# Kernel tuning notes

Hardware: AMD Instinct MI355X
Metric: run time of the kernel (lower is better)

## Reference

```python
import jax, jax.numpy as jnp
import numpy as np

B, S, D, N = 16, 1024, 512, 2048
SPECTRAL_RADIUS = 0.95
SPARSITY = 0.01  # effective_sparsity = max(0.01, 5/N) = 0.01 for N=2048


def setup_inputs() -> dict:
    key = jax.random.key(0)
    k_x, k_fb, k_wraw, k_mask, k_win, k_wfb = jax.random.split(key, 6)
    x_seq = jax.random.normal(k_x, (B, S, D), dtype=jnp.float32)
    feedback_seq = jax.random.normal(k_fb, (B, S, D), dtype=jnp.float32)
    initial_state = jnp.zeros((B, N), dtype=jnp.float32)
    # Fixed random reservoir: sparse gaussian rescaled to spectral radius ~0.95.
    # For an NxN gaussian with density p, spectral radius ~= sqrt(N*p), so we
    # rescale by SPECTRAL_RADIUS / sqrt(N*p) (the torch code uses the exact
    # max eigenvalue; this approximation preserves the same math structure).
    W_raw = jax.random.normal(k_wraw, (N, N), dtype=jnp.float32)
    mask = (jax.random.uniform(k_mask, (N, N)) < SPARSITY).astype(jnp.float32)
    W_res = W_raw * mask * (SPECTRAL_RADIUS / jnp.sqrt(N * SPARSITY))
    W_in = jax.random.normal(k_win, (N, D), dtype=jnp.float32) * 0.1
    W_fb = jax.random.normal(k_wfb, (N, D), dtype=jnp.float32) * 0.1
    return {
        "x_seq": x_seq,
        "feedback_seq": feedback_seq,
        "initial_state": initial_state,
        "W_res": W_res,
        "W_in": W_in,
        "W_fb": W_fb,
    }


def reference(x_seq, feedback_seq, initial_state, W_res, W_in, W_fb):
    # Precompute input + feedback projections as one batched GEMM each
    # (same math as per-step einsums: 'bi,ni->bn' == x @ W.T).
    drive = jnp.einsum("bsd,nd->sbn", x_seq, W_in) + jnp.einsum(
        "bsd,nd->sbn", feedback_seq, W_fb
    )  # (S, B, N)

    def step(state, drive_t):
        # pre = state @ W_res.T + W_in x_t + W_fb fb_t
        new_state = jnp.tanh(state @ W_res.T + drive_t)
        return new_state, new_state

    _, states = jax.lax.scan(step, initial_state, drive)  # (S, B, N)
    return jnp.transpose(states, (1, 0, 2))  # (B, S, N)
```

## Files before the change

### kernel.cpp

```cpp
#include <hip/hip_runtime.h>
#include <stdint.h>

typedef unsigned short u16;
typedef unsigned int   u32;
typedef __attribute__((ext_vector_type(8))) short short8;
typedef __attribute__((ext_vector_type(4))) float f32x4;

#define CAP   52
#define CAPW  26

__device__ __forceinline__ u16 rne_bf16(float f){
  u32 u = __float_as_uint(f);
  u32 r = (u + 0x7fffu + ((u >> 16) & 1u)) >> 16;
  return (u16)r;
}
__device__ __forceinline__ float bf16_to_f(u16 h){
  return __uint_as_float(((u32)h) << 16);
}
__device__ __forceinline__ float tanh_fast(float x){
  float e = __expf(2.0f * x);
  return 1.0f - 2.0f / (e + 1.0f);
}

__global__ __launch_bounds__(256) void pack_a_k(const float* __restrict__ x,
                                                const float* __restrict__ fb,
                                                u16* __restrict__ A){
  int idx = blockIdx.x * 256 + threadIdx.x;
  int m = idx >> 9, d = idx & 511;
  float xv = x[idx];
  float fv = fb[idx];
  u16 xh = rne_bf16(xv); u16 xl = rne_bf16(xv - bf16_to_f(xh));
  u16 fh = rne_bf16(fv); u16 fl = rne_bf16(fv - bf16_to_f(fh));
  size_t base = (size_t)m * 2048;
  A[base + d]        = xh;
  A[base + 512 + d]  = fh;
  A[base + 1024 + d] = xl;
  A[base + 1536 + d] = fl;
}

__global__ __launch_bounds__(256) void pack_b_k(const float* __restrict__ Win,
                                                const float* __restrict__ Wfb,
                                                u16* __restrict__ Bm){
  int idx = blockIdx.x * 256 + threadIdx.x;
  int n = idx >> 9, d = idx & 511;
  float iv = Win[idx];
  float fv = Wfb[idx];
  u16 ih = rne_bf16(iv); u16 il = rne_bf16(iv - bf16_to_f(ih));
  u16 fh = rne_bf16(fv); u16 fl = rne_bf16(fv - bf16_to_f(fh));
  size_t base = (size_t)n * 3072;
  Bm[base + d]        = ih;
  Bm[base + 512 + d]  = fh;
  Bm[base + 1024 + d] = ih;
  Bm[base + 1536 + d] = fh;
  Bm[base + 2048 + d] = il;
  Bm[base + 2560 + d] = fl;
}

#define GLDS(gp, lp) __builtin_amdgcn_global_load_lds( \
    (const __attribute__((address_space(1))) void*)(gp), \
    (__attribute__((address_space(3))) void*)(lp), 16, 0, 0)

__global__ __launch_bounds__(256) void gemm_k(const u16* __restrict__ A,
                                              const u16* __restrict__ Bm,
                                              float* __restrict__ C){
  __shared__ __align__(16) u16 As[128 * 32];
  __shared__ __align__(16) u16 Bs[128 * 32];
  const int tid = threadIdx.x;
  const int w = tid >> 6, l = tid & 63;
  const int bid = blockIdx.x;
  const int mt = bid >> 4, nt = bid & 15;
  const int m0 = mt * 128, n0 = nt * 128;
  const int srow = tid >> 2;
  const int scol = (tid & 3) * 8;
  const int wr = w & 1, wc = w >> 1;
  const int lhi = l >> 4, llo = l & 15;

  f32x4 acc[4][4];
  #pragma unroll
  for (int i = 0; i < 4; i++)
    #pragma unroll
    for (int j = 0; j < 4; j++)
      acc[i][j] = (f32x4){0.f, 0.f, 0.f, 0.f};

  for (int kt = 0; kt < 96; ++kt){
    int k = kt * 32;
    int keff = (k >= 2048) ? (k - 2048) : k;
    #pragma unroll
    for (int r = 0; r < 2; r++){
      const u16* ga = A  + (size_t)(m0 + r * 64 + srow) * 2048 + keff + scol;
      GLDS(ga, &As[r * 2048 + w * 512]);
      const u16* gb = Bm + (size_t)(n0 + r * 64 + srow) * 3072 + k + scol;
      GLDS(gb, &Bs[r * 2048 + w * 512]);
    }
    __syncthreads();
    short8 af[4], bf[4];
    #pragma unroll
    for (int i = 0; i < 4; i++){
      af[i] = *(const short8*)&As[(wr * 64 + i * 16 + llo) * 32 + lhi * 8];
      bf[i] = *(const short8*)&Bs[(wc * 64 + i * 16 + llo) * 32 + lhi * 8];
    }
    #pragma unroll
    for (int i = 0; i < 4; i++)
      #pragma unroll
      for (int j = 0; j < 4; j++)
        acc[i][j] = __builtin_amdgcn_mfma_f32_16x16x32_bf16(af[i], bf[j], acc[i][j], 0, 0, 0);
    __syncthreads();
  }
  #pragma unroll
  for (int i = 0; i < 4; i++)
    #pragma unroll
    for (int j = 0; j < 4; j++)
      #pragma unroll
      for (int rg = 0; rg < 4; rg++){
        int mr = m0 + wr * 64 + i * 16 + lhi * 4 + rg;
        int nc = n0 + wc * 64 + j * 16 + llo;
        C[(size_t)mr * 2048 + nc] = acc[i][j][rg];
      }
}

__global__ __launch_bounds__(256) void count_k(const float* __restrict__ W,
                                               int* __restrict__ nnz){
  int gt = blockIdx.x * 256 + threadIdx.x;
  int row = gt >> 6, l = gt & 63;
  const float* wr = W + (size_t)row * 2048;
  int c = 0;
  for (int i = 0; i < 32; i++) c += (wr[i * 64 + l] != 0.0f) ? 1 : 0;
  for (int off = 32; off; off >>= 1) c += __shfl_down(c, off, 64);
  if (l == 0) nnz[row] = c;
}

__global__ __launch_bounds__(1024) void sort_k(const int* __restrict__ nnz,
                                               u32* __restrict__ rowsp,
                                               int* __restrict__ L1a){
  __shared__ int hist[64], off[64], cur[64];
  __shared__ int order[2048];
  int tid = threadIdx.x;
  if (tid < 64){ hist[tid] = 0; cur[tid] = 0; }
  __syncthreads();
  for (int r = tid; r < 2048; r += 1024){
    int b = nnz[r]; if (b > 63) b = 63;
    atomicAdd(&hist[b], 1);
  }
  __syncthreads();
  if (tid == 0){
    int run = 0;
    for (int b = 63; b >= 0; b--){ off[b] = run; run += hist[b]; }
  }
  __syncthreads();
  for (int r = tid; r < 2048; r += 1024){
    int b = nnz[r]; if (b > 63) b = 63;
    int pos = off[b] + atomicAdd(&cur[b], 1);
    order[pos] = r;
  }
  __syncthreads();
  int rA = order[tid], rB = order[2047 - tid];
  rowsp[tid] = (u32)rA | ((u32)rB << 16);
  L1a[tid] = nnz[rA];
}

__global__ __launch_bounds__(256) void fill_k(const float* __restrict__ W,
                                              const u32* __restrict__ rowsp,
                                              float* __restrict__ valw,
                                              u32* __restrict__ col32){
  int gt = blockIdx.x * 256 + threadIdx.x;
  int p = gt >> 6, l = gt & 63;
  u32 rp = rowsp[p];
  int rA = (int)(rp & 0xffffu), rB = (int)(rp >> 16);
  int base = 0;
  for (int h = 0; h < 2; h++){
    int row = h ? rB : rA;
    const float* wr = W + (size_t)row * 2048;
    int cnt = 0;
    for (int i = 0; i < 32; i++){
      int c = i * 64 + l;
      float v = wr[c];
      unsigned long long m = __ballot(v != 0.0f);
      int pre = __popcll(m & ((1ull << l) - 1ull));
      if (v != 0.0f){
        int s = base + cnt + pre;
        if (s < CAP){
          valw[s * 1024 + p] = v;
          col32[s * 1024 + p] = (u32)c;
        }
      }
      cnt += __popcll(m);
    }
    base += cnt;
  }
  for (int s = base + l; s < CAP; s += 64){
    valw[s * 1024 + p] = 0.0f;
    col32[s * 1024 + p] = 0u;
  }
}

__global__ __launch_bounds__(256) void packc_k(const u32* __restrict__ c32,
                                               u32* __restrict__ cw){
  int idx = blockIdx.x * 256 + threadIdx.x;
  int j = idx >> 10, p = idx & 1023;
  cw[j * 1024 + p] = (c32[(2 * j) * 1024 + p] & 0xffffu) | (c32[(2 * j + 1) * 1024 + p] << 16);
}

__global__ __launch_bounds__(1024) void rnn_k(float* __restrict__ out,
                                              const float* __restrict__ init,
                                              const float* __restrict__ valw,
                                              const u32* __restrict__ cwg,
                                              const u32* __restrict__ rowsp,
                                              const int* __restrict__ L1a){
  const int tid = threadIdx.x, b = blockIdx.x;
  float val[CAP]; u32 cw[CAPW];
  #pragma unroll
  for (int k = 0; k < CAP; k++) val[k] = valw[k * 1024 + tid];
  #pragma unroll
  for (int j = 0; j < CAPW; j++) cw[j] = cwg[j * 1024 + tid];
  u32 rp = rowsp[tid];
  int rA = (int)(rp & 0xffffu), rB = (int)(rp >> 16);
  int L1 = L1a[tid];

  __shared__ float st[2048];
  st[tid]        = init[(size_t)b * 2048 + tid];
  st[tid + 1024] = init[(size_t)b * 2048 + tid + 1024];
  __syncthreads();

  float* ob = out + (size_t)b * 1024 * 2048;
  for (int t = 0; t < 1024; t++){
    float* orow = ob + (size_t)t * 2048;
    float dA = orow[rA];
    float dB = orow[rB];
    float aAll = 0.f, aA = 0.f;
    #pragma unroll
    for (int k = 0; k < CAP; k++){
      u32 col = (k & 1) ? (cw[k >> 1] >> 16) : (cw[k >> 1] & 0xffffu);
      float pv = val[k] * st[col];
      aAll += pv;
      aA += (k < L1) ? pv : 0.0f;
    }
    float aB = aAll - aA;
    __syncthreads();
    float sA = tanh_fast(aA + dA);
    float sB = tanh_fast(aB + dB);
    st[rA] = sA; st[rB] = sB;
    __syncthreads();
    orow[rA] = sA;
    orow[rB] = sB;
  }
}

extern "C" void kernel_launch(void* const* d_in, const int* in_sizes, int n_in,
                              void* d_out, int out_size, void* d_ws, size_t ws_size,
                              hipStream_t stream) {
  const float* x    = (const float*)d_in[0];
  const float* fb   = (const float*)d_in[1];
  const float* init = (const float*)d_in[2];
  const float* Wres = (const float*)d_in[3];
  const float* Win  = (const float*)d_in[4];
  const float* Wfb  = (const float*)d_in[5];
  float* out = (float*)d_out;

  char* w8 = (char*)d_ws;
  u16*  A_pack = (u16*)(w8);
  u16*  B_pack = (u16*)(w8 + 67108864);
  float* valw  = (float*)(w8 + 79691776);
  u32*  col32  = (u32*) (w8 + 79904768);
  u32*  colw   = (u32*) (w8 + 80117760);
  int*  nnz    = (int*) (w8 + 80224256);
  u32*  rowsp  = (u32*) (w8 + 80232448);
  int*  L1a    = (int*) (w8 + 80236544);

  pack_a_k<<<32768, 256, 0, stream>>>(x, fb, A_pack);
  pack_b_k<<<4096, 256, 0, stream>>>(Win, Wfb, B_pack);
  gemm_k<<<2048, 256, 0, stream>>>(A_pack, B_pack, out);
  count_k<<<512, 256, 0, stream>>>(Wres, nnz);
  sort_k<<<1, 1024, 0, stream>>>(nnz, rowsp, L1a);
  fill_k<<<256, 256, 0, stream>>>(Wres, rowsp, valw, col32);
  packc_k<<<(CAPW * 1024) / 256, 256, 0, stream>>>(col32, colw);
  rnn_k<<<16, 1024, 0, stream>>>(out, init, valw, colw, rowsp, L1a);
}
```

Measured before the change: 3.649 ms.

## Permute GEMM drive columns and bank-sort sparse columns for coalesced RNN access

```diff
diff --git a/kernel.cpp b/kernel.cpp
--- a/kernel.cpp
+++ b/kernel.cpp
@@ -62,6 +62,7 @@
 
 __global__ __launch_bounds__(256) void gemm_k(const u16* __restrict__ A,
                                               const u16* __restrict__ Bm,
+                                              const int* __restrict__ colmap,
                                               float* __restrict__ C){
   __shared__ __align__(16) u16 As[128 * 32];
   __shared__ __align__(16) u16 Bs[128 * 32];
@@ -106,6 +107,9 @@
         acc[i][j] = __builtin_amdgcn_mfma_f32_16x16x32_bf16(af[i], bf[j], acc[i][j], 0, 0, 0);
     __syncthreads();
   }
+  int cmj[4];
+  #pragma unroll
+  for (int j = 0; j < 4; j++) cmj[j] = colmap[n0 + wc * 64 + j * 16 + llo];
   #pragma unroll
   for (int i = 0; i < 4; i++)
     #pragma unroll
@@ -113,8 +117,7 @@
       #pragma unroll
       for (int rg = 0; rg < 4; rg++){
         int mr = m0 + wr * 64 + i * 16 + lhi * 4 + rg;
-        int nc = n0 + wc * 64 + j * 16 + llo;
-        C[(size_t)mr * 2048 + nc] = acc[i][j][rg];
+        C[(size_t)mr * 2048 + cmj[j]] = acc[i][j][rg];
       }
 }
 
@@ -131,7 +134,8 @@
 
 __global__ __launch_bounds__(1024) void sort_k(const int* __restrict__ nnz,
                                                u32* __restrict__ rowsp,
-                                               int* __restrict__ L1a){
+                                               int* __restrict__ L1a,
+                                               int* __restrict__ colmap){
   __shared__ int hist[64], off[64], cur[64];
   __shared__ int order[2048];
   int tid = threadIdx.x;
@@ -156,6 +160,8 @@
   int rA = order[tid], rB = order[2047 - tid];
   rowsp[tid] = (u32)rA | ((u32)rB << 16);
   L1a[tid] = nnz[rA];
+  colmap[rA] = tid;
+  colmap[rB] = tid + 1024;
 }
 
 __global__ __launch_bounds__(256) void fill_k(const float* __restrict__ W,
@@ -193,19 +199,51 @@
   }
 }
 
-__global__ __launch_bounds__(256) void packc_k(const u32* __restrict__ c32,
-                                               u32* __restrict__ cw){
-  int idx = blockIdx.x * 256 + threadIdx.x;
-  int j = idx >> 10, p = idx & 1023;
-  cw[j * 1024 + p] = (c32[(2 * j) * 1024 + p] & 0xffffu) | (c32[(2 * j + 1) * 1024 + p] << 16);
-}
-
-__global__ __launch_bounds__(1024) void rnn_k(float* __restrict__ out,
-                                              const float* __restrict__ init,
-                                              const float* __restrict__ valw,
-                                              const u32* __restrict__ cwg,
-                                              const u32* __restrict__ rowsp,
-                                              const int* __restrict__ L1a){
+__global__ __launch_bounds__(256) void reorder_k(const float* __restrict__ valw,
+                                                 const u32* __restrict__ col32,
+                                                 const int* __restrict__ L1a,
+                                                 float* __restrict__ val2,
+                                                 u32* __restrict__ cw2){
+  int p = blockIdx.x * 256 + threadIdx.x;
+  float v[CAP]; int c[CAP];
+  float tv[CAP]; int tc[CAP];
+  for (int k = 0; k < CAP; k++){ v[k] = valw[k * 1024 + p]; c[k] = (int)col32[k * 1024 + p]; }
+  int L1 = L1a[p];
+  int lane = p & 63;
+  int b0 = 0;
+  for (int s = 0; s < 2; s++){
+    int b1 = s ? CAP : L1;
+    int len = b1 - b0;
+    if (len > 0){
+      int cnt[32], st_[32], cur[32];
+      for (int b = 0; b < 32; b++){ cnt[b] = 0; cur[b] = 0; }
+      for (int i = b0; i < b1; i++) cnt[c[i] & 31]++;
+      int run = 0;
+      for (int b = 0; b < 32; b++){ st_[b] = run; run += cnt[b]; }
+      for (int i = b0; i < b1; i++){
+        int b = c[i] & 31;
+        int q = st_[b] + (cur[b]++);
+        tv[q] = v[i]; tc[q] = c[i];
+      }
+      int off = (lane * len) >> 6;
+      for (int q = 0; q < len; q++){
+        int src = q + off; if (src >= len) src -= len;
+        v[b0 + q] = tv[src]; c[b0 + q] = tc[src];
+      }
+    }
+    b0 = b1;
+  }
+  for (int k = 0; k < CAP; k++) val2[k * 1024 + p] = v[k];
+  for (int j = 0; j < CAPW; j++)
+    cw2[j * 1024 + p] = ((u32)(c[2 * j] << 2)) | (((u32)(c[2 * j + 1] << 2)) << 16);
+}
+
+__global__ __launch_bounds__(1024, 4) void rnn_k(float* __restrict__ out,
+                                                 const float* __restrict__ init,
+                                                 const float* __restrict__ valw,
+                                                 const u32* __restrict__ cwg,
+                                                 const u32* __restrict__ rowsp,
+                                                 const int* __restrict__ L1a){
   const int tid = threadIdx.x, b = blockIdx.x;
   float val[CAP]; u32 cw[CAPW];
   #pragma unroll
@@ -220,28 +258,31 @@
   st[tid]        = init[(size_t)b * 2048 + tid];
   st[tid + 1024] = init[(size_t)b * 2048 + tid + 1024];
   __syncthreads();
+  const char* stb = (const char*)st;
 
   float* ob = out + (size_t)b * 1024 * 2048;
   for (int t = 0; t < 1024; t++){
     float* orow = ob + (size_t)t * 2048;
-    float dA = orow[rA];
-    float dB = orow[rB];
+    float dA = orow[tid];
+    float dB = orow[tid + 1024];
     float aAll = 0.f, aA = 0.f;
     #pragma unroll
     for (int k = 0; k < CAP; k++){
-      u32 col = (k & 1) ? (cw[k >> 1] >> 16) : (cw[k >> 1] & 0xffffu);
-      float pv = val[k] * st[col];
+      u32 off = (k & 1) ? (cw[k >> 1] >> 16) : (cw[k >> 1] & 0xffffu);
+      float sv = *(const float*)(stb + off);
+      float pv = val[k] * sv;
       aAll += pv;
       aA += (k < L1) ? pv : 0.0f;
     }
-    float aB = aAll - aA;
+    float preA = aA + dA;
+    float preB = (aAll - aA) + dB;
     __syncthreads();
-    float sA = tanh_fast(aA + dA);
-    float sB = tanh_fast(aB + dB);
+    float sA = tanh_fast(preA);
+    float sB = tanh_fast(preB);
     st[rA] = sA; st[rB] = sB;
     __syncthreads();
-    orow[rA] = sA;
-    orow[rB] = sB;
+    orow[tid] = st[tid];
+    orow[tid + 1024] = st[tid + 1024];
   }
 }
 
@@ -261,17 +302,19 @@
   u16*  B_pack = (u16*)(w8 + 67108864);
   float* valw  = (float*)(w8 + 79691776);
   u32*  col32  = (u32*) (w8 + 79904768);
-  u32*  colw   = (u32*) (w8 + 80117760);
-  int*  nnz    = (int*) (w8 + 80224256);
-  u32*  rowsp  = (u32*) (w8 + 80232448);
-  int*  L1a    = (int*) (w8 + 80236544);
+  int*  colmap = (int*) (w8 + 80117760);
+  int*  nnz    = (int*) (w8 + 80125952);
+  u32*  rowsp  = (u32*) (w8 + 80134144);
+  int*  L1a    = (int*) (w8 + 80138240);
+  float* val2  = (float*)(w8);
+  u32*  cw2    = (u32*) (w8 + 212992);
 
   pack_a_k<<<32768, 256, 0, stream>>>(x, fb, A_pack);
   pack_b_k<<<4096, 256, 0, stream>>>(Win, Wfb, B_pack);
-  gemm_k<<<2048, 256, 0, stream>>>(A_pack, B_pack, out);
   count_k<<<512, 256, 0, stream>>>(Wres, nnz);
-  sort_k<<<1, 1024, 0, stream>>>(nnz, rowsp, L1a);
+  sort_k<<<1, 1024, 0, stream>>>(nnz, rowsp, L1a, colmap);
   fill_k<<<256, 256, 0, stream>>>(Wres, rowsp, valw, col32);
-  packc_k<<<(CAPW * 1024) / 256, 256, 0, stream>>>(col32, colw);
-  rnn_k<<<16, 1024, 0, stream>>>(out, init, valw, colw, rowsp, L1a);
-}
+  gemm_k<<<2048, 256, 0, stream>>>(A_pack, B_pack, colmap, out);
+  reorder_k<<<4, 256, 0, stream>>>(valw, col32, L1a, val2, cw2);
+  rnn_k<<<16, 1024, 0, stream>>>(out, init, val2, cw2, rowsp, L1a);
+}
```

Result: slower. 3.810 ms (+4.4%).

## Permute drive GEMM rows, pack weight+column into one word, coalesce recurrent I/O

Applied to the files above, without the earlier changes.

```diff
diff --git a/kernel.cpp b/kernel.cpp
--- a/kernel.cpp
+++ b/kernel.cpp
@@ -7,7 +7,6 @@
 typedef __attribute__((ext_vector_type(4))) float f32x4;
 
 #define CAP   52
-#define CAPW  26
 
 __device__ __forceinline__ u16 rne_bf16(float f){
   u32 u = __float_as_uint(f);
@@ -40,11 +39,13 @@
 
 __global__ __launch_bounds__(256) void pack_b_k(const float* __restrict__ Win,
                                                 const float* __restrict__ Wfb,
+                                                const int* __restrict__ rowperm,
                                                 u16* __restrict__ Bm){
   int idx = blockIdx.x * 256 + threadIdx.x;
   int n = idx >> 9, d = idx & 511;
-  float iv = Win[idx];
-  float fv = Wfb[idx];
+  int row = rowperm[n];
+  float iv = Win[(size_t)row * 512 + d];
+  float fv = Wfb[(size_t)row * 512 + d];
   u16 ih = rne_bf16(iv); u16 il = rne_bf16(iv - bf16_to_f(ih));
   u16 fh = rne_bf16(fv); u16 fl = rne_bf16(fv - bf16_to_f(fh));
   size_t base = (size_t)n * 3072;
@@ -131,7 +132,8 @@
 
 __global__ __launch_bounds__(1024) void sort_k(const int* __restrict__ nnz,
                                                u32* __restrict__ rowsp,
-                                               int* __restrict__ L1a){
+                                               int* __restrict__ L1a,
+                                               int* __restrict__ rowperm){
   __shared__ int hist[64], off[64], cur[64];
   __shared__ int order[2048];
   int tid = threadIdx.x;
@@ -156,12 +158,13 @@
   int rA = order[tid], rB = order[2047 - tid];
   rowsp[tid] = (u32)rA | ((u32)rB << 16);
   L1a[tid] = nnz[rA];
+  rowperm[tid] = rA;
+  rowperm[tid + 1024] = rB;
 }
 
 __global__ __launch_bounds__(256) void fill_k(const float* __restrict__ W,
                                               const u32* __restrict__ rowsp,
-                                              float* __restrict__ valw,
-                                              u32* __restrict__ col32){
+                                              u32* __restrict__ wpk){
   int gt = blockIdx.x * 256 + threadIdx.x;
   int p = gt >> 6, l = gt & 63;
   u32 rp = rowsp[p];
@@ -179,39 +182,30 @@
       if (v != 0.0f){
         int s = base + cnt + pre;
         if (s < CAP){
-          valw[s * 1024 + p] = v;
-          col32[s * 1024 + p] = (u32)c;
+          u32 u = __float_as_uint(v);
+          u = (u + 0x1000u) & 0xFFFFE000u;
+          wpk[s * 1024 + p] = u | ((u32)c << 2);
         }
       }
       cnt += __popcll(m);
     }
     base += cnt;
   }
-  for (int s = base + l; s < CAP; s += 64){
-    valw[s * 1024 + p] = 0.0f;
-    col32[s * 1024 + p] = 0u;
-  }
-}
-
-__global__ __launch_bounds__(256) void packc_k(const u32* __restrict__ c32,
-                                               u32* __restrict__ cw){
-  int idx = blockIdx.x * 256 + threadIdx.x;
-  int j = idx >> 10, p = idx & 1023;
-  cw[j * 1024 + p] = (c32[(2 * j) * 1024 + p] & 0xffffu) | (c32[(2 * j + 1) * 1024 + p] << 16);
-}
-
-__global__ __launch_bounds__(1024) void rnn_k(float* __restrict__ out,
-                                              const float* __restrict__ init,
-                                              const float* __restrict__ valw,
-                                              const u32* __restrict__ cwg,
-                                              const u32* __restrict__ rowsp,
-                                              const int* __restrict__ L1a){
+  for (int s = base + l; s < CAP; s += 64)
+    wpk[s * 1024 + p] = 0u;
+}
+
+__global__ __attribute__((amdgpu_flat_work_group_size(1024, 1024),
+                          amdgpu_waves_per_eu(4, 4)))
+void rnn_k(float* __restrict__ out,
+           const float* __restrict__ init,
+           const u32* __restrict__ wpkg,
+           const u32* __restrict__ rowsp,
+           const int* __restrict__ L1a){
   const int tid = threadIdx.x, b = blockIdx.x;
-  float val[CAP]; u32 cw[CAPW];
+  u32 wk[CAP];
   #pragma unroll
-  for (int k = 0; k < CAP; k++) val[k] = valw[k * 1024 + tid];
-  #pragma unroll
-  for (int j = 0; j < CAPW; j++) cw[j] = cwg[j * 1024 + tid];
+  for (int k = 0; k < CAP; k++) wk[k] = wpkg[k * 1024 + tid];
   u32 rp = rowsp[tid];
   int rA = (int)(rp & 0xffffu), rB = (int)(rp >> 16);
   int L1 = L1a[tid];
@@ -220,28 +214,35 @@
   st[tid]        = init[(size_t)b * 2048 + tid];
   st[tid + 1024] = init[(size_t)b * 2048 + tid + 1024];
   __syncthreads();
+  const char* stb = (const char*)st;
 
   float* ob = out + (size_t)b * 1024 * 2048;
+  float dA = __builtin_nontemporal_load(&ob[tid]);
+  float dB = __builtin_nontemporal_load(&ob[tid + 1024]);
   for (int t = 0; t < 1024; t++){
     float* orow = ob + (size_t)t * 2048;
-    float dA = orow[rA];
-    float dB = orow[rB];
+    const float* nrow = ob + (size_t)((t + 1) & 1023) * 2048;
+    float dA2 = __builtin_nontemporal_load(&nrow[tid]);
+    float dB2 = __builtin_nontemporal_load(&nrow[tid + 1024]);
     float aAll = 0.f, aA = 0.f;
     #pragma unroll
     for (int k = 0; k < CAP; k++){
-      u32 col = (k & 1) ? (cw[k >> 1] >> 16) : (cw[k >> 1] & 0xffffu);
-      float pv = val[k] * st[col];
+      u32 w = wk[k];
+      float sv = *(const float*)(stb + (w & 0x1FFCu));
+      float pv = __uint_as_float(w & 0xFFFFE000u) * sv;
       aAll += pv;
       aA += (k < L1) ? pv : 0.0f;
     }
-    float aB = aAll - aA;
-    __syncthreads();
-    float sA = tanh_fast(aA + dA);
-    float sB = tanh_fast(aB + dB);
+    float preA = aA + dA;
+    float preB = (aAll - aA) + dB;
+    __syncthreads();
+    float sA = tanh_fast(preA);
+    float sB = tanh_fast(preB);
     st[rA] = sA; st[rB] = sB;
     __syncthreads();
-    orow[rA] = sA;
-    orow[rB] = sB;
+    __builtin_nontemporal_store(st[tid], &orow[tid]);
+    __builtin_nontemporal_store(st[tid + 1024], &orow[tid + 1024]);
+    dA = dA2; dB = dB2;
   }
 }
 
@@ -259,19 +260,17 @@
   char* w8 = (char*)d_ws;
   u16*  A_pack = (u16*)(w8);
   u16*  B_pack = (u16*)(w8 + 67108864);
-  float* valw  = (float*)(w8 + 79691776);
-  u32*  col32  = (u32*) (w8 + 79904768);
-  u32*  colw   = (u32*) (w8 + 80117760);
-  int*  nnz    = (int*) (w8 + 80224256);
-  u32*  rowsp  = (u32*) (w8 + 80232448);
-  int*  L1a    = (int*) (w8 + 80236544);
+  u32*  wpk    = (u32*) (w8 + 79691776);
+  int*  nnz    = (int*) (w8 + 79904768);
+  u32*  rowsp  = (u32*) (w8 + 79912960);
+  int*  L1a    = (int*) (w8 + 79917056);
+  int*  rowperm= (int*) (w8 + 79921152);
 
   pack_a_k<<<32768, 256, 0, stream>>>(x, fb, A_pack);
-  pack_b_k<<<4096, 256, 0, stream>>>(Win, Wfb, B_pack);
+  count_k<<<512, 256, 0, stream>>>(Wres, nnz);
+  sort_k<<<1, 1024, 0, stream>>>(nnz, rowsp, L1a, rowperm);
+  pack_b_k<<<4096, 256, 0, stream>>>(Win, Wfb, rowperm, B_pack);
+  fill_k<<<256, 256, 0, stream>>>(Wres, rowsp, wpk);
   gemm_k<<<2048, 256, 0, stream>>>(A_pack, B_pack, out);
-  count_k<<<512, 256, 0, stream>>>(Wres, nnz);
-  sort_k<<<1, 1024, 0, stream>>>(nnz, rowsp, L1a);
-  fill_k<<<256, 256, 0, stream>>>(Wres, rowsp, valw, col32);
-  packc_k<<<(CAPW * 1024) / 256, 256, 0, stream>>>(col32, colw);
-  rnn_k<<<16, 1024, 0, stream>>>(out, init, valw, colw, rowsp, L1a);
-}
+  rnn_k<<<16, 1024, 0, stream>>>(out, init, wpk, rowsp, L1a);
+}
```

Measured after the change: 3.255 ms. -10.8%, faster.
